# Optimization experiments

Hardware: AMD Instinct MI355X
Metric: run time of the kernel (lower is better)

Reference implementation:

```python
import jax, jax.numpy as jnp
import numpy as np

ENC_DIM, DEC_DIM, ATT_DIM = 2048, 512, 512


def setup_inputs() -> dict:
    key = jax.random.key(0)
    ks = jax.random.split(key, 8)
    s = lambda d: 1.0 / np.sqrt(d)
    return {
        "encoder_features": jax.random.normal(ks[0], (256, ENC_DIM, 14, 14), jnp.float32),
        "decoder_hidden": jax.random.normal(ks[1], (256, DEC_DIM), jnp.float32),
        "W_enc": jax.random.uniform(ks[2], (ENC_DIM, ATT_DIM), jnp.float32, -s(ENC_DIM), s(ENC_DIM)),
        "b_enc": jax.random.uniform(ks[3], (ATT_DIM,), jnp.float32, -s(ENC_DIM), s(ENC_DIM)),
        "W_dec": jax.random.uniform(ks[4], (DEC_DIM, ATT_DIM), jnp.float32, -s(DEC_DIM), s(DEC_DIM)),
        "b_dec": jax.random.uniform(ks[5], (ATT_DIM,), jnp.float32, -s(DEC_DIM), s(DEC_DIM)),
        "W_full": jax.random.uniform(ks[6], (ATT_DIM, 1), jnp.float32, -s(ATT_DIM), s(ATT_DIM)),
        "b_full": jax.random.uniform(ks[7], (1,), jnp.float32, -s(ATT_DIM), s(ATT_DIM)),
    }


def reference(encoder_features, decoder_hidden, W_enc, b_enc, W_dec, b_dec, W_full, b_full):
    B, C, H, W = encoder_features.shape
    # [B, P, C] with P = H*W pixels
    feats = encoder_features.reshape(B, C, H * W).transpose(0, 2, 1)
    enc_att = jnp.einsum('bpc,ca->bpa', feats, W_enc) + b_enc            # [B,P,A]
    dec_att = decoder_hidden @ W_dec + b_dec                              # [B,A]
    att = jnp.einsum('bpa,a->bp', jax.nn.relu(enc_att + dec_att[:, None, :]), W_full[:, 0]) + b_full[0]
    alpha = jax.nn.softmax(att, axis=1)                                   # [B,P]
    context = jnp.einsum('bpc,bp->bc', feats, alpha)                      # [B,C]
    return (context, alpha)
```

## Files before the change

kernel.cpp:

```cpp
#include <hip/hip_runtime.h>

typedef unsigned short u16;
typedef __bf16 bf16x8 __attribute__((ext_vector_type(8)));
typedef float f32x4 __attribute__((ext_vector_type(4)));

#define B_   256
#define C_   2048
#define P_   196
#define A_   512
#define CP_  (C_ * P_)
#define MTOT (B_ * P_)

#define BM 128
#define BK 32

__device__ __forceinline__ u16 f2bf(float f) {
    unsigned int x = __float_as_uint(f);
    unsigned int r = (x + 0x7fffu + ((x >> 16) & 1u)) >> 16;
    return (u16)r;
}

__device__ __forceinline__ void gl_lds16(const void* g, void* l) {
    __builtin_amdgcn_global_load_lds(
        (const __attribute__((address_space(1))) unsigned int*)g,
        (__attribute__((address_space(3))) unsigned int*)l, 16, 0, 0);
}

__global__ __launch_bounds__(256) void k_transpose_wenc(const float* __restrict__ W,
                                                        u16* __restrict__ Wt) {
    __shared__ u16 tile[64][65];
    int t  = threadIdx.x;
    int cb = (blockIdx.x & 31) * 64;
    int ab = (blockIdx.x >> 5) * 64;
#pragma unroll
    for (int i = 0; i < 16; ++i) {
        int c = (t >> 6) + i * 4;
        int a = t & 63;
        tile[c][a] = f2bf(W[(size_t)(cb + c) * A_ + ab + a]);
    }
    __syncthreads();
#pragma unroll
    for (int i = 0; i < 16; ++i) {
        int a  = (t >> 6) + i * 4;
        int cl = t & 63;
        Wt[(size_t)(ab + a) * C_ + cb + cl] = tile[cl][a];
    }
}

__global__ __launch_bounds__(512) void k_dec_att(const float* __restrict__ dh,
                                                 const float* __restrict__ Wd,
                                                 const float* __restrict__ bd,
                                                 float* __restrict__ out) {
    __shared__ float hL[512];
    int b = blockIdx.x, t = threadIdx.x;
    hL[t] = dh[b * 512 + t];
    __syncthreads();
    float s = bd[t];
#pragma unroll 8
    for (int k = 0; k < 512; ++k) s = fmaf(hL[k], Wd[k * 512 + t], s);
    out[b * 512 + t] = s;
}

__global__ __launch_bounds__(1024, 4) void k_gemm_att(const float* __restrict__ enc,
                                                      const u16* __restrict__ Wt,
                                                      const float* __restrict__ dec_att,
                                                      const float* __restrict__ benc,
                                                      const float* __restrict__ wfull,
                                                      const float* __restrict__ bfull,
                                                      float* __restrict__ att) {
    __shared__ u16   As[2][8 * 512];
    __shared__ u16   Bs[2][32 * 512];
    __shared__ float decL[2][512];
    __shared__ float wL[512];
    __shared__ float att_part[8][128];

    const int t    = threadIdx.x;
    const int lane = t & 63;
    const int wv   = t >> 6;
    const int l16  = lane & 15;
    const int lq   = lane >> 4;
    const int row0 = blockIdx.x * BM;

    const int b0 = row0 / 196;
    const int b1 = (row0 + BM - 1) / 196;
    if (t < 512) {
        decL[0][t] = dec_att[b0 * 512 + t] + benc[t];
        wL[t] = wfull[t];
    } else {
        decL[1][t - 512] = dec_att[b1 * 512 + (t - 512)] + benc[t - 512];
    }

    const int kq = t & 7;
    const int pl = t >> 3;
    const int pg = row0 + pl;
    const int bb = pg / 196;
    const int pp = pg - bb * 196;
    const float* srcA = enc + (size_t)bb * CP_ + (size_t)(kq * 4) * P_ + pp;
    const int a_off = (pl >> 4) * 512 + ((pl & 15) + 16 * (kq >> 1)) * 8 + (kq & 1) * 4;

    const u16* srcB = Wt + (size_t)(wv * 2 * 16 + l16) * C_ + lq * 8;
    const int  b_off = (wv * 2) * 512 + lane * 8;

    const int wr = wv & 1;
    const int wa = wv >> 1;

    f32x4 acc[4][4] = {};

    float av[4];
#pragma unroll
    for (int j = 0; j < 4; ++j) av[j] = srcA[(size_t)j * P_];
    {
        unsigned int lo = (unsigned int)f2bf(av[0]) | ((unsigned int)f2bf(av[1]) << 16);
        unsigned int hi = (unsigned int)f2bf(av[2]) | ((unsigned int)f2bf(av[3]) << 16);
        *(unsigned long long*)&As[0][a_off] =
            (unsigned long long)lo | ((unsigned long long)hi << 32);
    }
    gl_lds16(srcB, &Bs[0][b_off]);
    gl_lds16(srcB + (size_t)16 * C_, &Bs[0][b_off + 512]);

    int p = 0;
    for (int k = 0; k < C_ / BK; ++k) {
        __syncthreads();
        if (k + 1 < C_ / BK) {
            const u16* sB = srcB + (k + 1) * BK;
            gl_lds16(sB, &Bs[p ^ 1][b_off]);
            gl_lds16(sB + (size_t)16 * C_, &Bs[p ^ 1][b_off + 512]);
            const float* sA = srcA + (size_t)(k + 1) * BK * P_;
#pragma unroll
            for (int j = 0; j < 4; ++j) av[j] = sA[(size_t)j * P_];
        }
        bf16x8 bfr[4];
#pragma unroll
        for (int tr = 0; tr < 4; ++tr)
            bfr[tr] = *(const bf16x8*)&As[p][(wr * 4 + tr) * 512 + lane * 8];
#pragma unroll
        for (int ta = 0; ta < 4; ++ta) {
            bf16x8 afr = *(const bf16x8*)&Bs[p][(wa * 4 + ta) * 512 + lane * 8];
#pragma unroll
            for (int tr = 0; tr < 4; ++tr)
                acc[ta][tr] = __builtin_amdgcn_mfma_f32_16x16x32_bf16(afr, bfr[tr],
                                                                      acc[ta][tr], 0, 0, 0);
        }
        if (k + 1 < C_ / BK) {
            unsigned int lo = (unsigned int)f2bf(av[0]) | ((unsigned int)f2bf(av[1]) << 16);
            unsigned int hi = (unsigned int)f2bf(av[2]) | ((unsigned int)f2bf(av[3]) << 16);
            *(unsigned long long*)&As[p ^ 1][a_off] =
                (unsigned long long)lo | ((unsigned long long)hi << 32);
        }
        p ^= 1;
    }

    const int col = l16, quad = lq;
#pragma unroll
    for (int tr = 0; tr < 4; ++tr) {
        int rgl = wr * 64 + tr * 16 + col;
        int rgg = row0 + rgl;
        int bi  = rgg / 196 - b0;
        float s = 0.0f;
#pragma unroll
        for (int ta = 0; ta < 4; ++ta)
#pragma unroll
            for (int rr = 0; rr < 4; ++rr) {
                int a_idx = wa * 64 + ta * 16 + quad * 4 + rr;
                float v = acc[ta][tr][rr] + decL[bi][a_idx];
                s = fmaf(fmaxf(v, 0.0f), wL[a_idx], s);
            }
        s += __shfl_xor(s, 16);
        s += __shfl_xor(s, 32);
        if (quad == 0) att_part[wa][rgl] = s;
    }
    __syncthreads();
    if (t < BM) {
        float s = bfull[0];
#pragma unroll
        for (int w = 0; w < 8; ++w) s += att_part[w][t];
        att[row0 + t] = s;
    }
}

__global__ __launch_bounds__(64) void k_softmax(const float* __restrict__ att,
                                                float* __restrict__ alpha) {
    int b = blockIdx.x, lane = threadIdx.x;
    const float* a = att + b * P_;
    float v[4];
    float mx = -__builtin_inff();
#pragma unroll
    for (int i = 0; i < 4; ++i) {
        int p = lane + i * 64;
        v[i] = (p < P_) ? a[p] : -__builtin_inff();
        mx = fmaxf(mx, v[i]);
    }
#pragma unroll
    for (int off = 32; off >= 1; off >>= 1) mx = fmaxf(mx, __shfl_xor(mx, off));
    float sum = 0.0f;
#pragma unroll
    for (int i = 0; i < 4; ++i) {
        int p = lane + i * 64;
        float e = (p < P_) ? expf(v[i] - mx) : 0.0f;
        v[i] = e;
        sum += e;
    }
#pragma unroll
    for (int off = 32; off >= 1; off >>= 1) sum += __shfl_xor(sum, off);
    float inv = 1.0f / sum;
#pragma unroll
    for (int i = 0; i < 4; ++i) {
        int p = lane + i * 64;
        if (p < P_) alpha[b * P_ + p] = v[i] * inv;
    }
}

__global__ __launch_bounds__(256) void k_context(const float* __restrict__ enc,
                                                 const float* __restrict__ alpha,
                                                 float* __restrict__ ctx) {
    __shared__ float aL[256];
    int t = threadIdx.x;
    int b = blockIdx.x >> 5;
    int chunk = blockIdx.x & 31;
    aL[t] = (t < P_) ? alpha[b * P_ + t] : 0.0f;
    __syncthreads();
    int wv = t >> 6, lane = t & 63;
    int cbase = chunk * 64 + wv * 16;
    const float* base = enc + (size_t)b * CP_;
#pragma unroll 4
    for (int i = 0; i < 16; ++i) {
        int c = cbase + i;
        float s = 0.0f;
        if (lane < 49) {
            float4 f = *(const float4*)(base + (size_t)c * P_ + lane * 4);
            float4 a4 = *(const float4*)&aL[lane * 4];
            s = f.x * a4.x + f.y * a4.y + f.z * a4.z + f.w * a4.w;
        }
#pragma unroll
        for (int off = 32; off >= 1; off >>= 1) s += __shfl_xor(s, off);
        if (lane == 0) ctx[(size_t)b * C_ + c] = s;
    }
}

extern "C" void kernel_launch(void* const* d_in, const int* in_sizes, int n_in,
                              void* d_out, int out_size, void* d_ws, size_t ws_size,
                              hipStream_t stream) {
    const float* enc   = (const float*)d_in[0];
    const float* dh    = (const float*)d_in[1];
    const float* Wenc  = (const float*)d_in[2];
    const float* benc  = (const float*)d_in[3];
    const float* Wdec  = (const float*)d_in[4];
    const float* bdec  = (const float*)d_in[5];
    const float* wfull = (const float*)d_in[6];
    const float* bfull = (const float*)d_in[7];

    u16*   Wt  = (u16*)d_ws;
    float* dec = (float*)((char*)d_ws + (2u << 20));
    float* att = (float*)((char*)d_ws + (2u << 20) + (512u << 10));

    float* ctx     = (float*)d_out;
    float* alpha_o = ctx + B_ * C_;

    k_transpose_wenc<<<dim3(256), dim3(256), 0, stream>>>(Wenc, Wt);
    k_dec_att<<<dim3(256), dim3(512), 0, stream>>>(dh, Wdec, bdec, dec);
    k_gemm_att<<<dim3(MTOT / BM), dim3(1024), 0, stream>>>(enc, Wt, dec, benc,
                                                           wfull, bfull, att);
    k_softmax<<<dim3(256), dim3(64), 0, stream>>>(att, alpha_o);
    k_context<<<dim3(256 * 32), dim3(256), 0, stream>>>(enc, alpha_o, ctx);
}
```

Measured before the change: 820.7 us.

## Shrink GEMM tile, load W_enc fragments directly to registers, restructure context reduction

The attention GEMM moves from a 128-row tile to a 64-row tile with 512 threads. Each wave owns 64 attention columns and loads its W_enc fragments straight from global memory into registers, replacing the LDS staging. The main loop is unrolled by two with explicit As ping-pong and a lightweight waitcnt+barrier, so the 1024-thread barrier sync and the LDS B buffer go away and more blocks can run at once. The context kernel now has each wave reduce four channels at a time using 16-lane groups, which cuts idle lanes and shuffle depth. The trade-off is that B fragments are re-read from global or L2 by twice as many blocks.

```diff
diff --git a/kernel.cpp b/kernel.cpp
--- a/kernel.cpp
+++ b/kernel.cpp
@@ -11,8 +11,9 @@
 #define CP_  (C_ * P_)
 #define MTOT (B_ * P_)
 
-#define BM 128
+#define BM 64
 #define BK 32
+#define NBLK (MTOT / BM)
 
 __device__ __forceinline__ u16 f2bf(float f) {
     unsigned int x = __float_as_uint(f);
@@ -20,11 +21,13 @@
     return (u16)r;
 }
 
-__device__ __forceinline__ void gl_lds16(const void* g, void* l) {
-    __builtin_amdgcn_global_load_lds(
-        (const __attribute__((address_space(1))) unsigned int*)g,
-        (__attribute__((address_space(3))) unsigned int*)l, 16, 0, 0);
-}
+__device__ __forceinline__ unsigned long long pack4bf(const float* v) {
+    unsigned int lo = (unsigned int)f2bf(v[0]) | ((unsigned int)f2bf(v[1]) << 16);
+    unsigned int hi = (unsigned int)f2bf(v[2]) | ((unsigned int)f2bf(v[3]) << 16);
+    return (unsigned long long)lo | ((unsigned long long)hi << 32);
+}
+
+#define WG_BARRIER() asm volatile("s_waitcnt lgkmcnt(0)\n\ts_barrier" ::: "memory")
 
 __global__ __launch_bounds__(256) void k_transpose_wenc(const float* __restrict__ W,
                                                         u16* __restrict__ Wt) {
@@ -61,34 +64,30 @@
     out[b * 512 + t] = s;
 }
 
-__global__ __launch_bounds__(1024, 4) void k_gemm_att(const float* __restrict__ enc,
-                                                      const u16* __restrict__ Wt,
-                                                      const float* __restrict__ dec_att,
-                                                      const float* __restrict__ benc,
-                                                      const float* __restrict__ wfull,
-                                                      const float* __restrict__ bfull,
-                                                      float* __restrict__ att) {
-    __shared__ u16   As[2][8 * 512];
-    __shared__ u16   Bs[2][32 * 512];
+__global__ __launch_bounds__(512, 4) void k_gemm_att(const float* __restrict__ enc,
+                                                     const u16* __restrict__ Wt,
+                                                     const float* __restrict__ dec_att,
+                                                     const float* __restrict__ benc,
+                                                     const float* __restrict__ wfull,
+                                                     const float* __restrict__ bfull,
+                                                     float* __restrict__ att) {
+    __shared__ u16   As[2][4 * 512];
     __shared__ float decL[2][512];
     __shared__ float wL[512];
-    __shared__ float att_part[8][128];
+    __shared__ float att_part[8][64];
 
     const int t    = threadIdx.x;
     const int lane = t & 63;
-    const int wv   = t >> 6;
+    const int wa   = t >> 6;
     const int l16  = lane & 15;
     const int lq   = lane >> 4;
     const int row0 = blockIdx.x * BM;
 
     const int b0 = row0 / 196;
     const int b1 = (row0 + BM - 1) / 196;
-    if (t < 512) {
-        decL[0][t] = dec_att[b0 * 512 + t] + benc[t];
-        wL[t] = wfull[t];
-    } else {
-        decL[1][t - 512] = dec_att[b1 * 512 + (t - 512)] + benc[t - 512];
-    }
+    decL[0][t] = dec_att[b0 * 512 + t] + benc[t];
+    decL[1][t] = dec_att[b1 * 512 + t] + benc[t];
+    wL[t] = wfull[t];
 
     const int kq = t & 7;
     const int pl = t >> 3;
@@ -98,64 +97,72 @@
     const float* srcA = enc + (size_t)bb * CP_ + (size_t)(kq * 4) * P_ + pp;
     const int a_off = (pl >> 4) * 512 + ((pl & 15) + 16 * (kq >> 1)) * 8 + (kq & 1) * 4;
 
-    const u16* srcB = Wt + (size_t)(wv * 2 * 16 + l16) * C_ + lq * 8;
-    const int  b_off = (wv * 2) * 512 + lane * 8;
-
-    const int wr = wv & 1;
-    const int wa = wv >> 1;
+    const u16* srcB = Wt + (size_t)(wa * 64 + l16) * C_ + lq * 8;
 
     f32x4 acc[4][4] = {};
 
-    float av[4];
-#pragma unroll
-    for (int j = 0; j < 4; ++j) av[j] = srcA[(size_t)j * P_];
-    {
-        unsigned int lo = (unsigned int)f2bf(av[0]) | ((unsigned int)f2bf(av[1]) << 16);
-        unsigned int hi = (unsigned int)f2bf(av[2]) | ((unsigned int)f2bf(av[3]) << 16);
-        *(unsigned long long*)&As[0][a_off] =
-            (unsigned long long)lo | ((unsigned long long)hi << 32);
-    }
-    gl_lds16(srcB, &Bs[0][b_off]);
-    gl_lds16(srcB + (size_t)16 * C_, &Bs[0][b_off + 512]);
-
-    int p = 0;
-    for (int k = 0; k < C_ / BK; ++k) {
-        __syncthreads();
-        if (k + 1 < C_ / BK) {
-            const u16* sB = srcB + (k + 1) * BK;
-            gl_lds16(sB, &Bs[p ^ 1][b_off]);
-            gl_lds16(sB + (size_t)16 * C_, &Bs[p ^ 1][b_off + 512]);
-            const float* sA = srcA + (size_t)(k + 1) * BK * P_;
-#pragma unroll
-            for (int j = 0; j < 4; ++j) av[j] = sA[(size_t)j * P_];
-        }
+    float av0[4], av1[4];
+#pragma unroll
+    for (int j = 0; j < 4; ++j) av0[j] = srcA[(size_t)j * P_];
+    *(unsigned long long*)&As[0][a_off] = pack4bf(av0);
+#pragma unroll
+    for (int j = 0; j < 4; ++j) av1[j] = srcA[(size_t)BK * P_ + (size_t)j * P_];
+    bf16x8 bcur[4];
+#pragma unroll
+    for (int ta = 0; ta < 4; ++ta)
+        bcur[ta] = *(const bf16x8*)(srcB + (size_t)(ta * 16) * C_);
+    WG_BARRIER();
+
+    for (int k = 0; k < C_ / BK; k += 2) {
         bf16x8 bfr[4];
 #pragma unroll
         for (int tr = 0; tr < 4; ++tr)
-            bfr[tr] = *(const bf16x8*)&As[p][(wr * 4 + tr) * 512 + lane * 8];
-#pragma unroll
-        for (int ta = 0; ta < 4; ++ta) {
-            bf16x8 afr = *(const bf16x8*)&Bs[p][(wa * 4 + ta) * 512 + lane * 8];
+            bfr[tr] = *(const bf16x8*)&As[0][tr * 512 + lane * 8];
+        if (k + 2 < C_ / BK) {
+#pragma unroll
+            for (int j = 0; j < 4; ++j)
+                av0[j] = srcA[(size_t)(k + 2) * BK * P_ + (size_t)j * P_];
+        }
+#pragma unroll
+        for (int ta = 0; ta < 4; ++ta)
 #pragma unroll
             for (int tr = 0; tr < 4; ++tr)
-                acc[ta][tr] = __builtin_amdgcn_mfma_f32_16x16x32_bf16(afr, bfr[tr],
+                acc[ta][tr] = __builtin_amdgcn_mfma_f32_16x16x32_bf16(bcur[ta], bfr[tr],
                                                                       acc[ta][tr], 0, 0, 0);
-        }
-        if (k + 1 < C_ / BK) {
-            unsigned int lo = (unsigned int)f2bf(av[0]) | ((unsigned int)f2bf(av[1]) << 16);
-            unsigned int hi = (unsigned int)f2bf(av[2]) | ((unsigned int)f2bf(av[3]) << 16);
-            *(unsigned long long*)&As[p ^ 1][a_off] =
-                (unsigned long long)lo | ((unsigned long long)hi << 32);
-        }
-        p ^= 1;
+#pragma unroll
+        for (int ta = 0; ta < 4; ++ta)
+            bcur[ta] = *(const bf16x8*)(srcB + (size_t)(ta * 16) * C_ + (size_t)(k + 1) * 32);
+        *(unsigned long long*)&As[1][a_off] = pack4bf(av1);
+        WG_BARRIER();
+
+#pragma unroll
+        for (int tr = 0; tr < 4; ++tr)
+            bfr[tr] = *(const bf16x8*)&As[1][tr * 512 + lane * 8];
+        if (k + 3 < C_ / BK) {
+#pragma unroll
+            for (int j = 0; j < 4; ++j)
+                av1[j] = srcA[(size_t)(k + 3) * BK * P_ + (size_t)j * P_];
+        }
+#pragma unroll
+        for (int ta = 0; ta < 4; ++ta)
+#pragma unroll
+            for (int tr = 0; tr < 4; ++tr)
+                acc[ta][tr] = __builtin_amdgcn_mfma_f32_16x16x32_bf16(bcur[ta], bfr[tr],
+                                                                      acc[ta][tr], 0, 0, 0);
+        if (k + 2 < C_ / BK) {
+#pragma unroll
+            for (int ta = 0; ta < 4; ++ta)
+                bcur[ta] = *(const bf16x8*)(srcB + (size_t)(ta * 16) * C_ + (size_t)(k + 2) * 32);
+            *(unsigned long long*)&As[0][a_off] = pack4bf(av0);
+        }
+        WG_BARRIER();
     }
 
     const int col = l16, quad = lq;
 #pragma unroll
     for (int tr = 0; tr < 4; ++tr) {
-        int rgl = wr * 64 + tr * 16 + col;
-        int rgg = row0 + rgl;
-        int bi  = rgg / 196 - b0;
+        int rgl = tr * 16 + col;
+        int bi  = (row0 + rgl) / 196 - b0;
         float s = 0.0f;
 #pragma unroll
         for (int ta = 0; ta < 4; ++ta)
@@ -213,27 +220,37 @@
 __global__ __launch_bounds__(256) void k_context(const float* __restrict__ enc,
                                                  const float* __restrict__ alpha,
                                                  float* __restrict__ ctx) {
-    __shared__ float aL[256];
+    __shared__ float aL[200];
     int t = threadIdx.x;
     int b = blockIdx.x >> 5;
     int chunk = blockIdx.x & 31;
-    aL[t] = (t < P_) ? alpha[b * P_ + t] : 0.0f;
-    __syncthreads();
-    int wv = t >> 6, lane = t & 63;
-    int cbase = chunk * 64 + wv * 16;
-    const float* base = enc + (size_t)b * CP_;
-#pragma unroll 4
-    for (int i = 0; i < 16; ++i) {
-        int c = cbase + i;
-        float s = 0.0f;
-        if (lane < 49) {
-            float4 f = *(const float4*)(base + (size_t)c * P_ + lane * 4);
-            float4 a4 = *(const float4*)&aL[lane * 4];
-            s = f.x * a4.x + f.y * a4.y + f.z * a4.z + f.w * a4.w;
-        }
-#pragma unroll
-        for (int off = 32; off >= 1; off >>= 1) s += __shfl_xor(s, off);
-        if (lane == 0) ctx[(size_t)b * C_ + c] = s;
+    if (t < P_) aL[t] = alpha[b * P_ + t];
+    __syncthreads();
+    int wv = t >> 6, l = t & 63, g = l >> 4, j = l & 15;
+    float4 a0 = *(const float4*)&aL[j * 4];
+    float4 a1 = *(const float4*)&aL[64 + j * 4];
+    float4 a2 = *(const float4*)&aL[128 + j * 4];
+    float4 a3 = *(const float4*)&aL[192];
+    const float* base = enc + (size_t)b * CP_ + (size_t)(chunk * 64) * P_;
+#pragma unroll
+    for (int pass = 0; pass < 4; ++pass) {
+        int r = wv * 16 + pass * 4 + g;
+        const float* row = base + (size_t)r * P_;
+        float4 f0 = *(const float4*)(row + j * 4);
+        float4 f1 = *(const float4*)(row + 64 + j * 4);
+        float4 f2 = *(const float4*)(row + 128 + j * 4);
+        float s = f0.x * a0.x + f0.y * a0.y + f0.z * a0.z + f0.w * a0.w;
+        s += f1.x * a1.x + f1.y * a1.y + f1.z * a1.z + f1.w * a1.w;
+        s += f2.x * a2.x + f2.y * a2.y + f2.z * a2.z + f2.w * a2.w;
+        if (j == 0) {
+            float4 f3 = *(const float4*)(row + 192);
+            s += f3.x * a3.x + f3.y * a3.y + f3.z * a3.z + f3.w * a3.w;
+        }
+        s += __shfl_xor(s, 1);
+        s += __shfl_xor(s, 2);
+        s += __shfl_xor(s, 4);
+        s += __shfl_xor(s, 8);
+        if (j == 0) ctx[(size_t)b * C_ + chunk * 64 + r] = s;
     }
 }
 
@@ -258,8 +275,8 @@
 
     k_transpose_wenc<<<dim3(256), dim3(256), 0, stream>>>(Wenc, Wt);
     k_dec_att<<<dim3(256), dim3(512), 0, stream>>>(dh, Wdec, bdec, dec);
-    k_gemm_att<<<dim3(MTOT / BM), dim3(1024), 0, stream>>>(enc, Wt, dec, benc,
-                                                           wfull, bfull, att);
+    k_gemm_att<<<dim3(NBLK), dim3(512), 0, stream>>>(enc, Wt, dec, benc,
+                                                     wfull, bfull, att);
     k_softmax<<<dim3(256), dim3(64), 0, stream>>>(att, alpha_o);
     k_context<<<dim3(256 * 32), dim3(256), 0, stream>>>(enc, alpha_o, ctx);
 }
```

Measured after the change: 905.9 us. 10.4% more time.

## Shrink GEMM row tile to 64 with 512 threads; restructure context reduction

Applied to the files above, without the earlier changes.

The attention GEMM now uses 64-row tiles with 512 threads. Each wave covers 64 attention columns across all 64 rows and loads four B sub-tiles per stage instead of two. This doubles the block count to fill the GPU better, but each row tile streams the full bf16 W_enc twice as often. The partial-sum buffer now reuses the A shared buffer. The context kernel is rewritten so 16-lane groups each reduce one channel row with three or four float4 loads, replacing the 49-of-64-lane layout and the full-wave shuffle reductions.

```diff
diff --git a/kernel.cpp b/kernel.cpp
--- a/kernel.cpp
+++ b/kernel.cpp
@@ -11,8 +11,9 @@
 #define CP_  (C_ * P_)
 #define MTOT (B_ * P_)
 
-#define BM 128
+#define BM 64
 #define BK 32
+#define NBLK (MTOT / BM)
 
 __device__ __forceinline__ u16 f2bf(float f) {
     unsigned int x = __float_as_uint(f);
@@ -61,18 +62,18 @@
     out[b * 512 + t] = s;
 }
 
-__global__ __launch_bounds__(1024, 4) void k_gemm_att(const float* __restrict__ enc,
-                                                      const u16* __restrict__ Wt,
-                                                      const float* __restrict__ dec_att,
-                                                      const float* __restrict__ benc,
-                                                      const float* __restrict__ wfull,
-                                                      const float* __restrict__ bfull,
-                                                      float* __restrict__ att) {
-    __shared__ u16   As[2][8 * 512];
+__global__ __launch_bounds__(512, 4) void k_gemm_att(const float* __restrict__ enc,
+                                                     const u16* __restrict__ Wt,
+                                                     const float* __restrict__ dec_att,
+                                                     const float* __restrict__ benc,
+                                                     const float* __restrict__ wfull,
+                                                     const float* __restrict__ bfull,
+                                                     float* __restrict__ att) {
+    __shared__ u16   As[2][4 * 512];
     __shared__ u16   Bs[2][32 * 512];
     __shared__ float decL[2][512];
     __shared__ float wL[512];
-    __shared__ float att_part[8][128];
+    float* att_part = (float*)&As[0][0];
 
     const int t    = threadIdx.x;
     const int lane = t & 63;
@@ -83,12 +84,9 @@
 
     const int b0 = row0 / 196;
     const int b1 = (row0 + BM - 1) / 196;
-    if (t < 512) {
-        decL[0][t] = dec_att[b0 * 512 + t] + benc[t];
-        wL[t] = wfull[t];
-    } else {
-        decL[1][t - 512] = dec_att[b1 * 512 + (t - 512)] + benc[t - 512];
-    }
+    decL[0][t] = dec_att[b0 * 512 + t] + benc[t];
+    decL[1][t] = dec_att[b1 * 512 + t] + benc[t];
+    wL[t] = wfull[t];
 
     const int kq = t & 7;
     const int pl = t >> 3;
@@ -98,11 +96,8 @@
     const float* srcA = enc + (size_t)bb * CP_ + (size_t)(kq * 4) * P_ + pp;
     const int a_off = (pl >> 4) * 512 + ((pl & 15) + 16 * (kq >> 1)) * 8 + (kq & 1) * 4;
 
-    const u16* srcB = Wt + (size_t)(wv * 2 * 16 + l16) * C_ + lq * 8;
-    const int  b_off = (wv * 2) * 512 + lane * 8;
-
-    const int wr = wv & 1;
-    const int wa = wv >> 1;
+    const u16* srcB  = Wt + (size_t)(wv * 64 + l16) * C_ + lq * 8;
+    const int  b_off = (wv * 4) * 512 + lane * 8;
 
     f32x4 acc[4][4] = {};
 
@@ -115,16 +110,20 @@
         *(unsigned long long*)&As[0][a_off] =
             (unsigned long long)lo | ((unsigned long long)hi << 32);
     }
-    gl_lds16(srcB, &Bs[0][b_off]);
+    gl_lds16(srcB,                   &Bs[0][b_off]);
     gl_lds16(srcB + (size_t)16 * C_, &Bs[0][b_off + 512]);
+    gl_lds16(srcB + (size_t)32 * C_, &Bs[0][b_off + 1024]);
+    gl_lds16(srcB + (size_t)48 * C_, &Bs[0][b_off + 1536]);
 
     int p = 0;
     for (int k = 0; k < C_ / BK; ++k) {
         __syncthreads();
         if (k + 1 < C_ / BK) {
-            const u16* sB = srcB + (k + 1) * BK;
-            gl_lds16(sB, &Bs[p ^ 1][b_off]);
+            const u16* sB = srcB + (size_t)(k + 1) * BK;
+            gl_lds16(sB,                   &Bs[p ^ 1][b_off]);
             gl_lds16(sB + (size_t)16 * C_, &Bs[p ^ 1][b_off + 512]);
+            gl_lds16(sB + (size_t)32 * C_, &Bs[p ^ 1][b_off + 1024]);
+            gl_lds16(sB + (size_t)48 * C_, &Bs[p ^ 1][b_off + 1536]);
             const float* sA = srcA + (size_t)(k + 1) * BK * P_;
 #pragma unroll
             for (int j = 0; j < 4; ++j) av[j] = sA[(size_t)j * P_];
@@ -132,10 +131,10 @@
         bf16x8 bfr[4];
 #pragma unroll
         for (int tr = 0; tr < 4; ++tr)
-            bfr[tr] = *(const bf16x8*)&As[p][(wr * 4 + tr) * 512 + lane * 8];
+            bfr[tr] = *(const bf16x8*)&As[p][tr * 512 + lane * 8];
 #pragma unroll
         for (int ta = 0; ta < 4; ++ta) {
-            bf16x8 afr = *(const bf16x8*)&Bs[p][(wa * 4 + ta) * 512 + lane * 8];
+            bf16x8 afr = *(const bf16x8*)&Bs[p][(wv * 4 + ta) * 512 + lane * 8];
 #pragma unroll
             for (int tr = 0; tr < 4; ++tr)
                 acc[ta][tr] = __builtin_amdgcn_mfma_f32_16x16x32_bf16(afr, bfr[tr],
@@ -153,27 +152,26 @@
     const int col = l16, quad = lq;
 #pragma unroll
     for (int tr = 0; tr < 4; ++tr) {
-        int rgl = wr * 64 + tr * 16 + col;
-        int rgg = row0 + rgl;
-        int bi  = rgg / 196 - b0;
+        int rgl = tr * 16 + col;
+        int bi  = (row0 + rgl) / 196 - b0;
         float s = 0.0f;
 #pragma unroll
         for (int ta = 0; ta < 4; ++ta)
 #pragma unroll
             for (int rr = 0; rr < 4; ++rr) {
-                int a_idx = wa * 64 + ta * 16 + quad * 4 + rr;
+                int a_idx = wv * 64 + ta * 16 + quad * 4 + rr;
                 float v = acc[ta][tr][rr] + decL[bi][a_idx];
                 s = fmaf(fmaxf(v, 0.0f), wL[a_idx], s);
             }
         s += __shfl_xor(s, 16);
         s += __shfl_xor(s, 32);
-        if (quad == 0) att_part[wa][rgl] = s;
+        if (quad == 0) att_part[wv * 64 + rgl] = s;
     }
     __syncthreads();
     if (t < BM) {
         float s = bfull[0];
 #pragma unroll
-        for (int w = 0; w < 8; ++w) s += att_part[w][t];
+        for (int w = 0; w < 8; ++w) s += att_part[w * 64 + t];
         att[row0 + t] = s;
     }
 }
@@ -213,27 +211,37 @@
 __global__ __launch_bounds__(256) void k_context(const float* __restrict__ enc,
                                                  const float* __restrict__ alpha,
                                                  float* __restrict__ ctx) {
-    __shared__ float aL[256];
+    __shared__ float aL[200];
     int t = threadIdx.x;
     int b = blockIdx.x >> 5;
     int chunk = blockIdx.x & 31;
-    aL[t] = (t < P_) ? alpha[b * P_ + t] : 0.0f;
-    __syncthreads();
-    int wv = t >> 6, lane = t & 63;
-    int cbase = chunk * 64 + wv * 16;
-    const float* base = enc + (size_t)b * CP_;
-#pragma unroll 4
-    for (int i = 0; i < 16; ++i) {
-        int c = cbase + i;
-        float s = 0.0f;
-        if (lane < 49) {
-            float4 f = *(const float4*)(base + (size_t)c * P_ + lane * 4);
-            float4 a4 = *(const float4*)&aL[lane * 4];
-            s = f.x * a4.x + f.y * a4.y + f.z * a4.z + f.w * a4.w;
-        }
-#pragma unroll
-        for (int off = 32; off >= 1; off >>= 1) s += __shfl_xor(s, off);
-        if (lane == 0) ctx[(size_t)b * C_ + c] = s;
+    if (t < P_) aL[t] = alpha[b * P_ + t];
+    __syncthreads();
+    int wv = t >> 6, l = t & 63, g = l >> 4, j = l & 15;
+    float4 a0 = *(const float4*)&aL[j * 4];
+    float4 a1 = *(const float4*)&aL[64 + j * 4];
+    float4 a2 = *(const float4*)&aL[128 + j * 4];
+    float4 a3 = *(const float4*)&aL[192];
+    const float* base = enc + (size_t)b * CP_ + (size_t)(chunk * 64) * P_;
+#pragma unroll
+    for (int pass = 0; pass < 4; ++pass) {
+        int r = wv * 16 + pass * 4 + g;
+        const float* row = base + (size_t)r * P_;
+        float4 f0 = *(const float4*)(row + j * 4);
+        float4 f1 = *(const float4*)(row + 64 + j * 4);
+        float4 f2 = *(const float4*)(row + 128 + j * 4);
+        float s = f0.x * a0.x + f0.y * a0.y + f0.z * a0.z + f0.w * a0.w;
+        s += f1.x * a1.x + f1.y * a1.y + f1.z * a1.z + f1.w * a1.w;
+        s += f2.x * a2.x + f2.y * a2.y + f2.z * a2.z + f2.w * a2.w;
+        if (j == 0) {
+            float4 f3 = *(const float4*)(row + 192);
+            s += f3.x * a3.x + f3.y * a3.y + f3.z * a3.z + f3.w * a3.w;
+        }
+        s += __shfl_xor(s, 1);
+        s += __shfl_xor(s, 2);
+        s += __shfl_xor(s, 4);
+        s += __shfl_xor(s, 8);
+        if (j == 0) ctx[(size_t)b * C_ + chunk * 64 + r] = s;
     }
 }
 
@@ -258,8 +266,8 @@
 
     k_transpose_wenc<<<dim3(256), dim3(256), 0, stream>>>(Wenc, Wt);
     k_dec_att<<<dim3(256), dim3(512), 0, stream>>>(dh, Wdec, bdec, dec);
-    k_gemm_att<<<dim3(MTOT / BM), dim3(1024), 0, stream>>>(enc, Wt, dec, benc,
-                                                           wfull, bfull, att);
+    k_gemm_att<<<dim3(NBLK), dim3(512), 0, stream>>>(enc, Wt, dec, benc,
+                                                     wfull, bfull, att);
     k_softmax<<<dim3(256), dim3(64), 0, stream>>>(att, alpha_o);
     k_context<<<dim3(256 * 32), dim3(256), 0, stream>>>(enc, alpha_o, ctx);
 }
```

Result: slower. 920.6 us (+12.2%).
